# Kernel tuning notes

Hardware: AMD Instinct MI355X
Metric: run time of the kernel (lower is better)

## Reference

```python
import jax, jax.numpy as jnp
import numpy as np

H = 8          # num_heads
SPARSITY = 0.1


def setup_inputs() -> dict:
    key = jax.random.key(0)
    ks = jax.random.split(key, 16)
    B, S, D = 2, 2048, 1024
    g2 = H * H  # 64, distill width
    std = 0.02
    inp = {
        "x":   jax.random.normal(ks[0], (B, S, D), dtype=jnp.float32),
        "Wq":  jax.random.normal(ks[1], (D, D)) * std, "bq": jnp.zeros((D,)),
        "Wk":  jax.random.normal(ks[2], (D, D)) * std, "bk": jnp.zeros((D,)),
        "Wv":  jax.random.normal(ks[3], (D, D)) * std, "bv": jnp.zeros((D,)),
        "Wo":  jax.random.normal(ks[4], (D, D)) * std, "bo": jnp.zeros((D,)),
        "Wd":  jax.random.normal(ks[5], (g2, g2)) * std, "bd": jnp.zeros((g2,)),
        "Wg":  jax.random.normal(ks[6], (g2, D)) * std,  "bg": jnp.zeros((g2,)),
        "Wgp": jax.random.normal(ks[7], (D, g2)) * std,  "bgp": jnp.zeros((D,)),
    }
    return inp


def reference(x, Wq, bq, Wk, bk, Wv, bv, Wo, bo, Wd, bd, Wg, bg, Wgp, bgp):
    B, S, D = x.shape
    Dh = D // H
    scale = Dh ** -0.5
    k = max(int(S * SPARSITY), 1)

    def heads(W, b):  # [B,S,D] -> [B,H,S,Dh]
        return (x @ W.T + b).reshape(B, S, H, Dh).transpose(0, 2, 1, 3)

    Q, K, V = heads(Wq, bq), heads(Wk, bk), heads(Wv, bv)

    scores = jnp.einsum("bhqd,bhkd->bhqk", Q, K) * scale       # [B,H,S,S]
    # per-row top-k threshold (k-th largest value of each query row)
    thr = jax.lax.top_k(scores, k)[0][..., k - 1:k]              # [B,H,S,1]
    masked = jnp.where(scores >= thr, scores, -jnp.inf)
    probs = jax.nn.softmax(masked, axis=-1)
    attn = jnp.einsum("bhqk,bhkd->bhqd", probs, V)               # [B,H,S,Dh]
    attn = attn.transpose(0, 2, 1, 3).reshape(B, S, D)           # [B,S,D]

    g2 = H * H
    distilled = (attn.reshape(-1, g2) @ Wd.T + bd).reshape(B, S, D)

    gate = jax.nn.sigmoid(x.mean(axis=1) @ Wg.T + bg)            # [B,g2]
    gate = (gate @ Wgp.T + bgp)[:, None, :]                      # [B,1,D]

    mixed = gate * distilled + (1.0 - gate) * attn
    return mixed @ Wo.T + bo
```

## Files before the change

kernel.cpp:

```cpp
#include <hip/hip_runtime.h>

typedef __attribute__((ext_vector_type(8))) short bf16x8;
typedef __attribute__((ext_vector_type(4))) float f32x4;
typedef __attribute__((ext_vector_type(4))) unsigned int u32x4;

#define DEVINL __device__ __forceinline__

DEVINL unsigned short f2bf(float f){
  unsigned int u = __float_as_uint(f);
  unsigned int r = (u + 0x7FFFu + ((u >> 16) & 1u)) >> 16;
  return (unsigned short)r;
}
DEVINL float bf2f(unsigned short h){ return __uint_as_float(((unsigned int)h) << 16); }
DEVINL unsigned int fkey(float f){
  unsigned int u = __float_as_uint(f);
  return (u & 0x80000000u) ? ~u : (u | 0x80000000u);
}
DEVINL float fkeyinv(unsigned int k){
  unsigned int u = (k & 0x80000000u) ? (k & 0x7FFFFFFFu) : ~k;
  return __uint_as_float(u);
}
DEVINL unsigned int cvtpk(float lo, float hi){
  unsigned int r;
  asm("v_cvt_pk_bf16_f32 %0, %1, %2" : "=v"(r) : "v"(lo), "v"(hi));
  return r;
}
DEVINL void gload16(void* lds, const void* g){
  __builtin_amdgcn_global_load_lds((const __attribute__((address_space(1))) void*)g,
                                   (__attribute__((address_space(3))) void*)lds, 16, 0, 0);
}

__global__ void prep_all_kernel(const float* __restrict__ x,
                                const float* __restrict__ Wq, const float* __restrict__ Wk,
                                const float* __restrict__ Wv,
                                unsigned short* __restrict__ xh, unsigned short* __restrict__ xl,
                                unsigned short* __restrict__ whi, unsigned short* __restrict__ wlo){
  const int NX = 4194304, NW = 1048576;
  int i = blockIdx.x * 256 + threadIdx.x;
  if (i < NX){
    float f = x[i];
    unsigned short h = f2bf(f);
    xh[i] = h; xl[i] = f2bf(f - bf2f(h));
  } else {
    int j = i - NX;
    const float* W = (j < NW) ? Wq : (j < 2*NW) ? Wk : Wv;
    int o = (j < NW) ? j : (j < 2*NW) ? (j - NW) : (j - 2*NW);
    float f = W[o];
    unsigned short h = f2bf(f);
    whi[j] = h; wlo[j] = f2bf(f - bf2f(h));
  }
}

__global__ void prep_split_kernel(const float* __restrict__ src,
                                  unsigned short* __restrict__ hi,
                                  unsigned short* __restrict__ lo, int n){
  int i = blockIdx.x * 256 + threadIdx.x;
  if (i >= n) return;
  float f = src[i];
  unsigned short h = f2bf(f);
  hi[i] = h;
  if (lo) lo[i] = f2bf(f - bf2f(h));
}

template<bool SPLIT, int EPI>
__global__ __launch_bounds__(256) void gemm_kernel(
    const unsigned short* __restrict__ Ah, const unsigned short* __restrict__ Al,
    const unsigned short* __restrict__ Bh, const unsigned short* __restrict__ Bl,
    const float* __restrict__ bias0, const float* __restrict__ bias1, const float* __restrict__ bias2,
    unsigned short* __restrict__ qh, unsigned short* __restrict__ ql,
    unsigned short* __restrict__ kh, unsigned short* __restrict__ kl,
    unsigned short* __restrict__ vT, float* __restrict__ outf)
{
  const int K = 1024;
  __shared__ __align__(16) unsigned short sAh[128*32];
  __shared__ __align__(16) unsigned short sBh[128*32];
  __shared__ __align__(16) unsigned short sAl[SPLIT ? 128*32 : 8];
  __shared__ __align__(16) unsigned short sBl[SPLIT ? 128*32 : 8];

  const int tid = threadIdx.x;
  const int lane = tid & 63;
  const int w = tid >> 6;
  const int wr = w >> 1, wc = w & 1;
  const int l16 = lane & 15, lg = lane >> 4;
  const int bm = blockIdx.x, bn = blockIdx.y;

  const int srow = (lane >> 2);
  const int scol = (lane & 3) * 8;
  const int r0 = w * 32;

  f32x4 acc[4][4];
  #pragma unroll
  for (int i = 0; i < 4; i++)
    #pragma unroll
    for (int j = 0; j < 4; j++)
      acc[i][j] = (f32x4){0.f,0.f,0.f,0.f};

  for (int kt = 0; kt < K/32; ++kt){
    __syncthreads();
    #pragma unroll
    for (int cc = 0; cc < 2; cc++){
      const int rr = r0 + cc*16 + srow;
      const int lb = (r0 + cc*16) * 32;
      gload16(&sAh[lb], &Ah[(size_t)(bm*128 + rr)*K + kt*32 + scol]);
      gload16(&sBh[lb], &Bh[(size_t)(bn*128 + rr)*K + kt*32 + scol]);
      if constexpr (SPLIT){
        gload16(&sAl[lb], &Al[(size_t)(bm*128 + rr)*K + kt*32 + scol]);
        gload16(&sBl[lb], &Bl[(size_t)(bn*128 + rr)*K + kt*32 + scol]);
      }
    }
    __syncthreads();

    bf16x8 afh[4], afl[4], bfh[4], bfl[4];
    #pragma unroll
    for (int mi = 0; mi < 4; mi++){
      int off = (wr*64 + mi*16 + l16)*32 + lg*8;
      afh[mi] = *(const bf16x8*)&sAh[off];
      if constexpr (SPLIT) afl[mi] = *(const bf16x8*)&sAl[off];
    }
    #pragma unroll
    for (int ni = 0; ni < 4; ni++){
      int off = (wc*64 + ni*16 + l16)*32 + lg*8;
      bfh[ni] = *(const bf16x8*)&sBh[off];
      if constexpr (SPLIT) bfl[ni] = *(const bf16x8*)&sBl[off];
    }
    #pragma unroll
    for (int mi = 0; mi < 4; mi++)
      #pragma unroll
      for (int ni = 0; ni < 4; ni++){
        acc[mi][ni] = __builtin_amdgcn_mfma_f32_16x16x32_bf16(afh[mi], bfh[ni], acc[mi][ni], 0, 0, 0);
        if constexpr (SPLIT){
          acc[mi][ni] = __builtin_amdgcn_mfma_f32_16x16x32_bf16(afh[mi], bfl[ni], acc[mi][ni], 0, 0, 0);
          acc[mi][ni] = __builtin_amdgcn_mfma_f32_16x16x32_bf16(afl[mi], bfh[ni], acc[mi][ni], 0, 0, 0);
        }
      }
  }

  if constexpr (EPI == 0){
    const int wsel = (bn * 128) >> 10;
    const float* bias = (wsel == 0) ? bias0 : (wsel == 1) ? bias1 : bias2;
    #pragma unroll
    for (int mi = 0; mi < 4; mi++)
      #pragma unroll
      for (int ni = 0; ni < 4; ni++)
        #pragma unroll
        for (int i = 0; i < 4; i++){
          int m = bm*128 + wr*64 + mi*16 + lg*4 + i;
          int ng = bn*128 + wc*64 + ni*16 + l16;
          int n = ng & 1023;
          float v = acc[mi][ni][i] + bias[n];
          int b = m >> 11, s = m & 2047;
          int h = n >> 7, dh = n & 127;
          size_t base = (size_t)(b*8 + h)*262144;
          if (wsel == 2){
            size_t off = base + (size_t)(s>>5)*4096 + (dh>>4)*512
                       + (size_t)((((s>>3)&3)*16 + (dh&15))*8 + (s&7));
            vT[off] = f2bf(v);
          } else {
            size_t off = base + (size_t)(s>>4)*2048 + (dh>>5)*512
                       + (size_t)((((dh>>3)&3)*16 + (s&15))*8 + (dh&7));
            unsigned short hv = f2bf(v);
            if (wsel == 0){ qh[off] = hv; ql[off] = f2bf(v - bf2f(hv)); }
            else          { kh[off] = hv; kl[off] = f2bf(v - bf2f(hv)); }
          }
        }
  } else {
    #pragma unroll
    for (int mi = 0; mi < 4; mi++)
      #pragma unroll
      for (int ni = 0; ni < 4; ni++)
        #pragma unroll
        for (int i = 0; i < 4; i++){
          int m = bm*128 + wr*64 + mi*16 + lg*4 + i;
          int n = bn*128 + wc*64 + ni*16 + l16;
          outf[(size_t)m*1024 + n] = acc[mi][ni][i] + bias0[n];
        }
  }
}

__global__ __launch_bounds__(512, 4) void attn_kernel(
    const unsigned short* __restrict__ qh, const unsigned short* __restrict__ ql,
    const unsigned short* __restrict__ kh, const unsigned short* __restrict__ kl,
    const unsigned short* __restrict__ vT, float* __restrict__ attn_out)
{
  __shared__ __align__(16) float red[8][16][132];
  __shared__ float rpartm[8][16], rpartd[8][16];
  __shared__ unsigned int prefixv[16], kremv[16];
  unsigned int* hist = (unsigned int*)red;

  const int tid = threadIdx.x;
  const int lane = tid & 63;
  const int w = tid >> 6;
  const int l16 = lane & 15, lg = lane >> 4;
  const int swz = (blockIdx.x & 7) * 256 + (blockIdx.x >> 3);
  const int bh = swz >> 7, qb = swz & 127;
  const float scale = 0.08838834764831845f;

  const size_t base = (size_t)bh*262144;

  const size_t qpb = base + (size_t)qb*2048 + lane*8;
  bf16x8 aqh[4], aql[4];
  #pragma unroll
  for (int kk = 0; kk < 4; kk++){
    aqh[kk] = *(const bf16x8*)&qh[qpb + kk*512];
    aql[kk] = *(const bf16x8*)&ql[qpb + kk*512];
  }

  f32x4 acc[16];
  #pragma unroll
  for (int nt = 0; nt < 16; nt++){
    f32x4 a0 = (f32x4){0.f,0.f,0.f,0.f};
    f32x4 a1 = (f32x4){0.f,0.f,0.f,0.f};
    const size_t kb = base + (size_t)(w*16 + nt)*2048 + lane*8;
    __builtin_amdgcn_s_setprio(1);
    #pragma unroll
    for (int kk = 0; kk < 4; kk++){
      bf16x8 kbh = *(const bf16x8*)&kh[kb + kk*512];
      bf16x8 kbl = *(const bf16x8*)&kl[kb + kk*512];
      a0 = __builtin_amdgcn_mfma_f32_16x16x32_bf16(kbh, aqh[kk], a0, 0, 0, 0);
      a1 = __builtin_amdgcn_mfma_f32_16x16x32_bf16(kbh, aql[kk], a1, 0, 0, 0);
      a1 = __builtin_amdgcn_mfma_f32_16x16x32_bf16(kbl, aqh[kk], a1, 0, 0, 0);
    }
    __builtin_amdgcn_s_setprio(0);
    #pragma unroll
    for (int i = 0; i < 4; i++) acc[nt][i] = (a0[i] + a1[i]) * scale;
  }

  {
    float rm = -3.4e38f;
    #pragma unroll
    for (int nt = 0; nt < 16; nt++)
      #pragma unroll
      for (int i = 0; i < 4; i++) rm = fmaxf(rm, acc[nt][i]);
    rm = fmaxf(rm, __shfl_xor(rm, 16, 64));
    rm = fmaxf(rm, __shfl_xor(rm, 32, 64));
    if (lane < 16) rpartm[w][lane] = rm;
  }
  if (tid < 16){ prefixv[tid] = 0u; kremv[tid] = 204u; }

  #pragma unroll
  for (int nt = 0; nt < 16; nt++)
    #pragma unroll
    for (int i = 0; i < 4; i++)
      acc[nt][i] = __uint_as_float(fkey(acc[nt][i]));

  const int hco = (w >> 1) * (16*257);
  for (int pass = 3; pass >= 0; pass--){
    const int shift = pass*8;
    __syncthreads();
    for (int j = tid; j < 4*16*257; j += 512) hist[j] = 0u;
    __syncthreads();
    const unsigned int pf = prefixv[l16];
    const unsigned int mhi = (pass == 3) ? 0u : (0xFFFFFFFFu << (shift + 8));
    #pragma unroll
    for (int nt = 0; nt < 16; nt++)
      #pragma unroll
      for (int i = 0; i < 4; i++){
        unsigned int u = __float_as_uint(acc[nt][i]);
        if ((u & mhi) == pf)
          atomicAdd(&hist[hco + l16*257 + ((u >> shift) & 255u)], 1u);
      }
    __syncthreads();
    #pragma unroll
    for (int rr = 0; rr < 2; rr++){
      int r = w*2 + rr;
      unsigned int krem = kremv[r];
      unsigned int pfx  = prefixv[r];
      unsigned int cl[4], s4 = 0;
      #pragma unroll
      for (int t = 0; t < 4; t++){
        int idx = r*257 + 255 - 4*lane - t;
        cl[t] = hist[idx] + hist[16*257 + idx] + hist[2*16*257 + idx] + hist[3*16*257 + idx];
        s4 += cl[t];
      }
      unsigned int inc = s4;
      #pragma unroll
      for (int off = 1; off < 64; off <<= 1){
        unsigned int v = __shfl_up((int)inc, off, 64);
        if (lane >= off) inc += v;
      }
      unsigned int cb = inc - s4;
      #pragma unroll
      for (int t = 0; t < 4; t++){
        if (krem > cb && krem <= cb + cl[t]){
          int d = 255 - 4*lane - t;
          prefixv[r] = pfx | ((unsigned int)d << shift);
          kremv[r]   = krem - cb;
        }
        cb += cl[t];
      }
    }
  }
  __syncthreads();

  const unsigned int th = prefixv[l16];
  float rmax = rpartm[0][l16];
  #pragma unroll
  for (int w8 = 1; w8 < 8; w8++) rmax = fmaxf(rmax, rpartm[w8][l16]);
  const int src01 = ((lg & 1) << 5) + l16;
  const int src23 = src01 + 16;
  const size_t vb0 = base + (size_t)(w*8)*4096 + lane*8;
  float dn = 0.f;
  f32x4 pacc[8];
  #pragma unroll
  for (int dt = 0; dt < 8; dt++) pacc[dt] = (f32x4){0.f,0.f,0.f,0.f};
  #pragma unroll
  for (int t = 0; t < 8; t++){
    float p[8];
    #pragma unroll
    for (int j = 0; j < 4; j++){
      unsigned int u = __float_as_uint(acc[2*t][j]);
      p[j] = (u >= th) ? __expf(fkeyinv(u) - rmax) : 0.f;
    }
    #pragma unroll
    for (int j = 0; j < 4; j++){
      unsigned int u = __float_as_uint(acc[2*t+1][j]);
      p[4+j] = (u >= th) ? __expf(fkeyinv(u) - rmax) : 0.f;
    }
    unsigned int d0 = cvtpk(p[0], p[1]), d1 = cvtpk(p[2], p[3]);
    unsigned int d2 = cvtpk(p[4], p[5]), d3 = cvtpk(p[6], p[7]);
    dn += __uint_as_float(d0 << 16) + __uint_as_float(d0 & 0xFFFF0000u)
        + __uint_as_float(d1 << 16) + __uint_as_float(d1 & 0xFFFF0000u)
        + __uint_as_float(d2 << 16) + __uint_as_float(d2 & 0xFFFF0000u)
        + __uint_as_float(d3 << 16) + __uint_as_float(d3 & 0xFFFF0000u);
    unsigned int A0 = (unsigned int)__shfl((int)d0, src01, 64);
    unsigned int A1 = (unsigned int)__shfl((int)d1, src01, 64);
    unsigned int A2 = (unsigned int)__shfl((int)d0, src23, 64);
    unsigned int A3 = (unsigned int)__shfl((int)d1, src23, 64);
    unsigned int B0 = (unsigned int)__shfl((int)d2, src01, 64);
    unsigned int B1 = (unsigned int)__shfl((int)d3, src01, 64);
    unsigned int B2 = (unsigned int)__shfl((int)d2, src23, 64);
    unsigned int B3 = (unsigned int)__shfl((int)d3, src23, 64);
    u32x4 pdv = (lg < 2) ? (u32x4){A0, A1, A2, A3} : (u32x4){B0, B1, B2, B3};
    bf16x8 pa = __builtin_bit_cast(bf16x8, pdv);
    __builtin_amdgcn_s_setprio(1);
    #pragma unroll
    for (int dt = 0; dt < 8; dt++){
      bf16x8 bv = *(const bf16x8*)&vT[vb0 + (size_t)t*4096 + dt*512];
      pacc[dt] = __builtin_amdgcn_mfma_f32_16x16x32_bf16(pa, bv, pacc[dt], 0, 0, 0);
    }
    __builtin_amdgcn_s_setprio(0);
  }
  dn += __shfl_xor(dn, 16, 64);
  dn += __shfl_xor(dn, 32, 64);
  if (lane < 16) rpartd[w][lane] = dn;

  #pragma unroll
  for (int dt = 0; dt < 8; dt++)
    #pragma unroll
    for (int i = 0; i < 4; i++)
      red[w][lg*4 + i][dt*16 + l16] = pacc[dt][i];
  __syncthreads();

  {
    const int q = tid >> 5;
    const int c0 = (tid & 31) * 4;
    f32x4 s0 = (f32x4){0.f,0.f,0.f,0.f};
    #pragma unroll
    for (int w8 = 0; w8 < 8; w8++)
      s0 += *(const f32x4*)&red[w8][q][c0];
    float dnm = 0.f;
    #pragma unroll
    for (int w8 = 0; w8 < 8; w8++) dnm += rpartd[w8][q];
    const int b = bh >> 3, h = bh & 7;
    float* op = &attn_out[((size_t)b*2048 + qb*16 + q)*1024 + h*128 + c0];
    f32x4 o0;
    #pragma unroll
    for (int i = 0; i < 4; i++) o0[i] = s0[i] / dnm;
    *(f32x4*)op = o0;
  }
}

__global__ void mean_partial_kernel(const float* __restrict__ x, float* __restrict__ partial){
  int b = blockIdx.x >> 7, ch = blockIdx.x & 127;
  int tid = threadIdx.x;
  #pragma unroll
  for (int dc = 0; dc < 4; dc++){
    int d = dc*256 + tid;
    float s = 0.f;
    for (int ss = 0; ss < 16; ss++) s += x[((size_t)b*2048 + ch*16 + ss)*1024 + d];
    partial[((size_t)b*128 + ch)*1024 + d] = s;
  }
}

__global__ __launch_bounds__(512) void gate_kernel2(const float* __restrict__ partial,
    const float* __restrict__ Wg, const float* __restrict__ bg,
    const float* __restrict__ Wgp, const float* __restrict__ bgp, float* __restrict__ gate){
  __shared__ float xm[1024];
  __shared__ float gb[64];
  const int b = blockIdx.x;
  const int tid = threadIdx.x, lane = tid & 63, w = tid >> 6;
  for (int d = tid; d < 1024; d += 512){
    float s = 0.f;
    for (int c = 0; c < 128; c++) s += partial[((size_t)b*128 + c)*1024 + d];
    xm[d] = s * (1.f/2048.f);
  }
  __syncthreads();
  for (int jj = 0; jj < 8; jj++){
    const int j = w*8 + jj;
    float s = 0.f;
    #pragma unroll
    for (int c = 0; c < 4; c++){
      f32x4 wv = *(const f32x4*)&Wg[(size_t)j*1024 + lane*16 + c*4];
      s += wv[0]*xm[lane*16 + c*4] + wv[1]*xm[lane*16 + c*4 + 1]
         + wv[2]*xm[lane*16 + c*4 + 2] + wv[3]*xm[lane*16 + c*4 + 3];
    }
    #pragma unroll
    for (int off = 1; off < 64; off <<= 1) s += __shfl_xor(s, off, 64);
    if (lane == 0) gb[j] = 1.f / (1.f + __expf(-(s + bg[j])));
  }
  __syncthreads();
  for (int d = tid; d < 1024; d += 512){
    float s = bgp[d];
    #pragma unroll
    for (int j4 = 0; j4 < 16; j4++){
      f32x4 wv = *(const f32x4*)&Wgp[(size_t)d*64 + j4*4];
      s += wv[0]*gb[j4*4] + wv[1]*gb[j4*4+1] + wv[2]*gb[j4*4+2] + wv[3]*gb[j4*4+3];
    }
    gate[b*1024 + d] = s;
  }
}

__global__ __launch_bounds__(256) void mix_kernel(const float* __restrict__ attn,
    const float* __restrict__ Wd, const float* __restrict__ bd,
    const float* __restrict__ gate,
    unsigned short* __restrict__ mixedh, unsigned short* __restrict__ mixedl){
  __shared__ float sWdT[64*64];
  __shared__ float arow[1024];
  int tid = threadIdx.x;
  for (int i = tid; i < 4096; i += 256){
    int m = i >> 6, cc = i & 63;
    sWdT[i] = Wd[cc*64 + m];
  }
  int rbase = blockIdx.x * 16;
  for (int rr = 0; rr < 16; rr++){
    int row = rbase + rr;
    __syncthreads();
    for (int i = tid; i < 1024; i += 256) arow[i] = attn[(size_t)row*1024 + i];
    __syncthreads();
    int b = row >> 11;
    #pragma unroll
    for (int c4 = 0; c4 < 4; c4++){
      int dcol = c4*256 + tid;
      int j = dcol >> 6, cc = dcol & 63;
      float y = bd[cc];
      for (int m = 0; m < 64; m++) y += arow[j*64 + m] * sWdT[m*64 + cc];
      float g = gate[b*1024 + dcol];
      float mv = g*y + (1.f - g)*arow[dcol];
      unsigned short hv = f2bf(mv);
      mixedh[(size_t)row*1024 + dcol] = hv;
      mixedl[(size_t)row*1024 + dcol] = f2bf(mv - bf2f(hv));
    }
  }
}

extern "C" void kernel_launch(void* const* d_in, const int* in_sizes, int n_in,
                              void* d_out, int out_size, void* d_ws, size_t ws_size,
                              hipStream_t stream){
  (void)in_sizes; (void)n_in; (void)out_size; (void)ws_size;
  const float* x   = (const float*)d_in[0];
  const float* Wq  = (const float*)d_in[1];
  const float* bq  = (const float*)d_in[2];
  const float* Wk  = (const float*)d_in[3];
  const float* bk  = (const float*)d_in[4];
  const float* Wv  = (const float*)d_in[5];
  const float* bv  = (const float*)d_in[6];
  const float* Wo  = (const float*)d_in[7];
  const float* bo  = (const float*)d_in[8];
  const float* Wd  = (const float*)d_in[9];
  const float* bd  = (const float*)d_in[10];
  const float* Wg  = (const float*)d_in[11];
  const float* bg  = (const float*)d_in[12];
  const float* Wgp = (const float*)d_in[13];
  const float* bgp = (const float*)d_in[14];
  float* out = (float*)d_out;

  const size_t MiB = 1048576;
  char* ws = (char*)d_ws;
  unsigned short* xh     = (unsigned short*)(ws + 0*MiB);
  unsigned short* xl     = (unsigned short*)(ws + 8*MiB);
  float*          attnws = (float*)(ws + 0*MiB);
  unsigned short* whi    = (unsigned short*)(ws + 16*MiB);
  unsigned short* wlo    = (unsigned short*)(ws + 22*MiB);
  unsigned short* wohi   = (unsigned short*)(ws + 16*MiB);
  unsigned short* wolo   = (unsigned short*)(ws + 18*MiB);
  float*          partial= (float*)(ws + 20*MiB);
  float*          gatews = (float*)(ws + 21*MiB);
  unsigned short* qh_    = (unsigned short*)(ws + 28*MiB);
  unsigned short* ql_    = (unsigned short*)(ws + 36*MiB);
  unsigned short* mixedh = (unsigned short*)(ws + 28*MiB);
  unsigned short* mixedl = (unsigned short*)(ws + 36*MiB);
  unsigned short* kh_    = (unsigned short*)(ws + 44*MiB);
  unsigned short* kl_    = (unsigned short*)(ws + 52*MiB);
  unsigned short* vT_    = (unsigned short*)(ws + 60*MiB);

  prep_all_kernel<<<28672, 256, 0, stream>>>(x, Wq, Wk, Wv, xh, xl, whi, wlo);

  gemm_kernel<true, 0><<<dim3(32, 24), 256, 0, stream>>>(
      xh, xl, whi, wlo, bq, bk, bv, qh_, ql_, kh_, kl_, vT_, nullptr);

  prep_split_kernel<<<4096, 256, 0, stream>>>(Wo, wohi, wolo, 1048576);
  mean_partial_kernel<<<256, 256, 0, stream>>>(x, partial);
  gate_kernel2<<<2, 512, 0, stream>>>(partial, Wg, bg, Wgp, bgp, gatews);

  attn_kernel<<<2048, 512, 0, stream>>>(qh_, ql_, kh_, kl_, vT_, attnws);

  mix_kernel<<<256, 256, 0, stream>>>(attnws, Wd, bd, gatews, mixedh, mixedl);

  gemm_kernel<true, 1><<<dim3(32, 8), 256, 0, stream>>>(
      mixedh, mixedl, wohi, wolo, bo, nullptr, nullptr,
      nullptr, nullptr, nullptr, nullptr, nullptr, out);
}
```

Baseline: 471.4 us.

## Stage QKV GEMM epilogue through shared memory and tune attention, mix kernels

The QKV projection epilogue now writes each output tile into shared memory in the permuted layout and then stores it with coalesced 16-byte writes, replacing scattered 2-byte stores. This needs a larger shared buffer and extra barriers. The attention kernel switches its address math from 64-bit to 32-bit, unrolls the radix-select pass loop, and clears the histogram with vector stores. The mix kernel gets twice as many blocks, each handling half as many rows, to improve occupancy.

```diff
diff --git a/kernel.cpp b/kernel.cpp
--- a/kernel.cpp
+++ b/kernel.cpp
@@ -62,7 +62,7 @@
   if (lo) lo[i] = f2bf(f - bf2f(h));
 }
 
-template<bool SPLIT, int EPI>
+template<int EPI>
 __global__ __launch_bounds__(256) void gemm_kernel(
     const unsigned short* __restrict__ Ah, const unsigned short* __restrict__ Al,
     const unsigned short* __restrict__ Bh, const unsigned short* __restrict__ Bl,
@@ -72,10 +72,11 @@
     unsigned short* __restrict__ vT, float* __restrict__ outf)
 {
   const int K = 1024;
-  __shared__ __align__(16) unsigned short sAh[128*32];
-  __shared__ __align__(16) unsigned short sBh[128*32];
-  __shared__ __align__(16) unsigned short sAl[SPLIT ? 128*32 : 8];
-  __shared__ __align__(16) unsigned short sBl[SPLIT ? 128*32 : 8];
+  __shared__ __align__(16) unsigned short smem[17408];
+  unsigned short* sAh = smem;
+  unsigned short* sBh = smem + 4096;
+  unsigned short* sAl = smem + 8192;
+  unsigned short* sBl = smem + 12288;
 
   const int tid = threadIdx.x;
   const int lane = tid & 63;
@@ -103,10 +104,8 @@
       const int lb = (r0 + cc*16) * 32;
       gload16(&sAh[lb], &Ah[(size_t)(bm*128 + rr)*K + kt*32 + scol]);
       gload16(&sBh[lb], &Bh[(size_t)(bn*128 + rr)*K + kt*32 + scol]);
-      if constexpr (SPLIT){
-        gload16(&sAl[lb], &Al[(size_t)(bm*128 + rr)*K + kt*32 + scol]);
-        gload16(&sBl[lb], &Bl[(size_t)(bn*128 + rr)*K + kt*32 + scol]);
-      }
+      gload16(&sAl[lb], &Al[(size_t)(bm*128 + rr)*K + kt*32 + scol]);
+      gload16(&sBl[lb], &Bl[(size_t)(bn*128 + rr)*K + kt*32 + scol]);
     }
     __syncthreads();
 
@@ -115,54 +114,66 @@
     for (int mi = 0; mi < 4; mi++){
       int off = (wr*64 + mi*16 + l16)*32 + lg*8;
       afh[mi] = *(const bf16x8*)&sAh[off];
-      if constexpr (SPLIT) afl[mi] = *(const bf16x8*)&sAl[off];
+      afl[mi] = *(const bf16x8*)&sAl[off];
     }
     #pragma unroll
     for (int ni = 0; ni < 4; ni++){
       int off = (wc*64 + ni*16 + l16)*32 + lg*8;
       bfh[ni] = *(const bf16x8*)&sBh[off];
-      if constexpr (SPLIT) bfl[ni] = *(const bf16x8*)&sBl[off];
+      bfl[ni] = *(const bf16x8*)&sBl[off];
     }
     #pragma unroll
     for (int mi = 0; mi < 4; mi++)
       #pragma unroll
       for (int ni = 0; ni < 4; ni++){
         acc[mi][ni] = __builtin_amdgcn_mfma_f32_16x16x32_bf16(afh[mi], bfh[ni], acc[mi][ni], 0, 0, 0);
-        if constexpr (SPLIT){
-          acc[mi][ni] = __builtin_amdgcn_mfma_f32_16x16x32_bf16(afh[mi], bfl[ni], acc[mi][ni], 0, 0, 0);
-          acc[mi][ni] = __builtin_amdgcn_mfma_f32_16x16x32_bf16(afl[mi], bfh[ni], acc[mi][ni], 0, 0, 0);
-        }
+        acc[mi][ni] = __builtin_amdgcn_mfma_f32_16x16x32_bf16(afh[mi], bfl[ni], acc[mi][ni], 0, 0, 0);
+        acc[mi][ni] = __builtin_amdgcn_mfma_f32_16x16x32_bf16(afl[mi], bfh[ni], acc[mi][ni], 0, 0, 0);
       }
   }
 
   if constexpr (EPI == 0){
     const int wsel = (bn * 128) >> 10;
     const float* bias = (wsel == 0) ? bias0 : (wsel == 1) ? bias1 : bias2;
-    #pragma unroll
-    for (int mi = 0; mi < 4; mi++)
-      #pragma unroll
-      for (int ni = 0; ni < 4; ni++)
+    const int h = bn & 7;
+    const unsigned rbase = (unsigned)(((bm >> 4)*8 + h)*262144) + (unsigned)((bm & 15)*16384);
+    const int nrounds = (wsel == 2) ? 1 : 2;
+    __syncthreads();
+    for (int arr = 0; arr < nrounds; arr++){
+      unsigned short* dst = (wsel == 0) ? (arr ? ql : qh)
+                          : (wsel == 1) ? (arr ? kl : kh) : vT;
+      #pragma unroll
+      for (int mi = 0; mi < 4; mi++)
         #pragma unroll
-        for (int i = 0; i < 4; i++){
-          int m = bm*128 + wr*64 + mi*16 + lg*4 + i;
-          int ng = bn*128 + wc*64 + ni*16 + l16;
-          int n = ng & 1023;
-          float v = acc[mi][ni][i] + bias[n];
-          int b = m >> 11, s = m & 2047;
-          int h = n >> 7, dh = n & 127;
-          size_t base = (size_t)(b*8 + h)*262144;
-          if (wsel == 2){
-            size_t off = base + (size_t)(s>>5)*4096 + (dh>>4)*512
-                       + (size_t)((((s>>3)&3)*16 + (dh&15))*8 + (s&7));
-            vT[off] = f2bf(v);
-          } else {
-            size_t off = base + (size_t)(s>>4)*2048 + (dh>>5)*512
-                       + (size_t)((((dh>>3)&3)*16 + (s&15))*8 + (dh&7));
+        for (int ni = 0; ni < 4; ni++)
+          #pragma unroll
+          for (int i = 0; i < 4; i++){
+            int s_local = wr*64 + mi*16 + lg*4 + i;
+            int dh = wc*64 + ni*16 + l16;
+            float v = acc[mi][ni][i] + bias[h*128 + dh];
             unsigned short hv = f2bf(v);
-            if (wsel == 0){ qh[off] = hv; ql[off] = f2bf(v - bf2f(hv)); }
-            else          { kh[off] = hv; kl[off] = f2bf(v - bf2f(hv)); }
+            unsigned short val = arr ? f2bf(v - bf2f(hv)) : hv;
+            if (wsel == 2) smem[dh*136 + s_local] = val;
+            else           smem[s_local*136 + dh] = val;
           }
+      __syncthreads();
+      #pragma unroll
+      for (int p = 0; p < 8; p++){
+        const int e0 = (p*256 + tid)*8;
+        int a;
+        if (wsel == 2){
+          int s0 = ((e0 >> 12) << 5) + (((e0 >> 7) & 3) << 3);
+          int dh = (((e0 >> 9) & 7) << 4) + ((e0 >> 3) & 15);
+          a = dh*136 + s0;
+        } else {
+          int s   = ((e0 >> 11) << 4) + ((e0 >> 3) & 15);
+          int dhs = (((e0 >> 9) & 3) << 5) + (((e0 >> 7) & 3) << 3);
+          a = s*136 + dhs;
         }
+        *(u32x4*)&dst[rbase + (unsigned)e0] = *(const u32x4*)&smem[a];
+      }
+      if (arr + 1 < nrounds) __syncthreads();
+    }
   } else {
     #pragma unroll
     for (int mi = 0; mi < 4; mi++)
@@ -195,9 +206,9 @@
   const int bh = swz >> 7, qb = swz & 127;
   const float scale = 0.08838834764831845f;
 
-  const size_t base = (size_t)bh*262144;
-
-  const size_t qpb = base + (size_t)qb*2048 + lane*8;
+  const unsigned base = (unsigned)bh * 262144u;
+
+  const unsigned qpb = base + (unsigned)qb*2048u + (unsigned)lane*8u;
   bf16x8 aqh[4], aql[4];
   #pragma unroll
   for (int kk = 0; kk < 4; kk++){
@@ -210,7 +221,7 @@
   for (int nt = 0; nt < 16; nt++){
     f32x4 a0 = (f32x4){0.f,0.f,0.f,0.f};
     f32x4 a1 = (f32x4){0.f,0.f,0.f,0.f};
-    const size_t kb = base + (size_t)(w*16 + nt)*2048 + lane*8;
+    const unsigned kb = base + (unsigned)(w*16 + nt)*2048u + (unsigned)lane*8u;
     __builtin_amdgcn_s_setprio(1);
     #pragma unroll
     for (int kk = 0; kk < 4; kk++){
@@ -244,10 +255,14 @@
       acc[nt][i] = __uint_as_float(fkey(acc[nt][i]));
 
   const int hco = (w >> 1) * (16*257);
+  #pragma unroll
   for (int pass = 3; pass >= 0; pass--){
     const int shift = pass*8;
     __syncthreads();
-    for (int j = tid; j < 4*16*257; j += 512) hist[j] = 0u;
+    {
+      const u32x4 z4 = (u32x4){0u,0u,0u,0u};
+      for (int j4 = tid; j4 < 4112; j4 += 512) *(u32x4*)&hist[j4*4] = z4;
+    }
     __syncthreads();
     const unsigned int pf = prefixv[l16];
     const unsigned int mhi = (pass == 3) ? 0u : (0xFFFFFFFFu << (shift + 8));
@@ -298,7 +313,7 @@
   for (int w8 = 1; w8 < 8; w8++) rmax = fmaxf(rmax, rpartm[w8][l16]);
   const int src01 = ((lg & 1) << 5) + l16;
   const int src23 = src01 + 16;
-  const size_t vb0 = base + (size_t)(w*8)*4096 + lane*8;
+  const unsigned vb0 = base + (unsigned)(w*8)*4096u + (unsigned)lane*8u;
   float dn = 0.f;
   f32x4 pacc[8];
   #pragma unroll
@@ -335,7 +350,7 @@
     __builtin_amdgcn_s_setprio(1);
     #pragma unroll
     for (int dt = 0; dt < 8; dt++){
-      bf16x8 bv = *(const bf16x8*)&vT[vb0 + (size_t)t*4096 + dt*512];
+      bf16x8 bv = *(const bf16x8*)&vT[vb0 + (unsigned)t*4096u + (unsigned)dt*512u];
       pacc[dt] = __builtin_amdgcn_mfma_f32_16x16x32_bf16(pa, bv, pacc[dt], 0, 0, 0);
     }
     __builtin_amdgcn_s_setprio(0);
@@ -431,8 +446,8 @@
     int m = i >> 6, cc = i & 63;
     sWdT[i] = Wd[cc*64 + m];
   }
-  int rbase = blockIdx.x * 16;
-  for (int rr = 0; rr < 16; rr++){
+  int rbase = blockIdx.x * 8;
+  for (int rr = 0; rr < 8; rr++){
     int row = rbase + rr;
     __syncthreads();
     for (int i = tid; i < 1024; i += 256) arow[i] = attn[(size_t)row*1024 + i];
@@ -495,7 +510,7 @@
 
   prep_all_kernel<<<28672, 256, 0, stream>>>(x, Wq, Wk, Wv, xh, xl, whi, wlo);
 
-  gemm_kernel<true, 0><<<dim3(32, 24), 256, 0, stream>>>(
+  gemm_kernel<0><<<dim3(32, 24), 256, 0, stream>>>(
       xh, xl, whi, wlo, bq, bk, bv, qh_, ql_, kh_, kl_, vT_, nullptr);
 
   prep_split_kernel<<<4096, 256, 0, stream>>>(Wo, wohi, wolo, 1048576);
@@ -504,9 +519,9 @@
 
   attn_kernel<<<2048, 512, 0, stream>>>(qh_, ql_, kh_, kl_, vT_, attnws);
 
-  mix_kernel<<<256, 256, 0, stream>>>(attnws, Wd, bd, gatews, mixedh, mixedl);
-
-  gemm_kernel<true, 1><<<dim3(32, 8), 256, 0, stream>>>(
+  mix_kernel<<<512, 256, 0, stream>>>(attnws, Wd, bd, gatews, mixedh, mixedl);
+
+  gemm_kernel<1><<<dim3(32, 8), 256, 0, stream>>>(
       mixedh, mixedl, wohi, wolo, bo, nullptr, nullptr,
       nullptr, nullptr, nullptr, nullptr, nullptr, out);
 }
```

Result: slower. 600.1 us (+27.3%).
